# Performance work log

Hardware: AMD Instinct MI355X
Metric: run time of the kernel (lower is better)

The kernel has to match this reference:

```python
import jax, jax.numpy as jnp
import numpy as np

B, Z, D, V, IN, R = 4, 128, 2, 2, 512, 256


def setup_inputs() -> dict:
    key = jax.random.key(0)
    ks = jax.random.split(key, 9)
    scale = 1.0 / np.sqrt(IN)
    inp = {
        "x1": jax.random.normal(ks[0], (B, Z, D, V, IN), jnp.float32),
        "x2": jax.random.normal(ks[1], (B, Z, D, V, IN), jnp.float32),
        "x3": jax.random.normal(ks[2], (B, Z, D, V, IN), jnp.float32),
        "W1": jax.random.normal(ks[3], (IN, R), jnp.float32) * scale,
        "b1": jax.random.normal(ks[4], (R,), jnp.float32) * scale,
        "W2": jax.random.normal(ks[5], (IN, R), jnp.float32) * scale,
        "b2": jax.random.normal(ks[6], (R,), jnp.float32) * scale,
        "W3": jax.random.normal(ks[7], (IN, R), jnp.float32) * scale,
        "b3": jax.random.normal(ks[8], (R,), jnp.float32) * scale,
    }
    return inp


def reference(x1, x2, x3, W1, b1, W2, b2, W3, b3):
    # Linear projections: [b, pos, d, v, in] @ [in, r] -> [b, pos, d, v, r]
    p1 = jnp.einsum('bzdvi,ir->bzdvr', x1, W1) + b1
    p2 = jnp.einsum('bxdvi,ir->bxdvr', x2, W2) + b2
    p3 = jnp.einsum('bcdvi,ir->bcdvr', x3, W3) + b3
    # Trilinear contraction over the factorized rank r, broadcasting over d, v
    return jnp.einsum('bzdve,bxdve,bcdve->bzxcdv', p1, p2, p3)
```

## Files before the change

### kernel.cpp

```cpp
#include <hip/hip_runtime.h>
#include <hip/hip_bf16.h>


typedef _Float16 f16;
typedef __attribute__((ext_vector_type(8)))  _Float16 f16x8;
typedef __attribute__((ext_vector_type(4)))  float    f32x4;
typedef __attribute__((ext_vector_type(16))) float    f32x16;

__global__ __launch_bounds__(256) void proj_kernel(
    const float* __restrict__ x1, const float* __restrict__ x2, const float* __restrict__ x3,
    const float* __restrict__ W1, const float* __restrict__ b1,
    const float* __restrict__ W2, const float* __restrict__ b2,
    const float* __restrict__ W3, const float* __restrict__ b3,
    f16* __restrict__ p1, f16* __restrict__ p2, f16* __restrict__ p3) {
    const int mat = blockIdx.z;
    const float* __restrict__ x    = (mat == 0) ? x1 : (mat == 1) ? x2 : x3;
    const float* __restrict__ W    = (mat == 0) ? W1 : (mat == 1) ? W2 : W3;
    const float* __restrict__ bias = (mat == 0) ? b1 : (mat == 1) ? b2 : b3;
    f16* __restrict__ p = (mat == 0) ? p1 : (mat == 1) ? p2 : p3;

    const int tid  = threadIdx.x;
    const int lane = tid & 63;
    const int w    = tid >> 6;
    const int ln   = lane & 31;
    const int kq   = lane >> 5;
    const int m0   = blockIdx.x * 64 + (w >> 1) * 32;
    const int n0b  = blockIdx.y * 64;
    const int n0   = n0b + (w & 1) * 32;

    __shared__ f16 sWt[64 * 40];

    f32x16 acc;
#pragma unroll
    for (int i = 0; i < 16; ++i) acc[i] = 0.f;

    const int snn = tid & 63, skk0 = tid >> 6;

#pragma unroll 1
    for (int ch = 0; ch < 16; ++ch) {
        const int k0 = ch * 32;
#pragma unroll
        for (int j = 0; j < 8; ++j) {
            const int kk = skk0 + 4 * j;
            sWt[snn * 40 + kk] = (f16)W[(size_t)(k0 + kk) * 256 + n0b + snn];
        }
        __syncthreads();
#pragma unroll
        for (int ks = 0; ks < 2; ++ks) {
            const float* X = x + (size_t)(m0 + ln) * 512 + k0 + ks * 16 + kq * 8;
            f32x4 a0 = *(const f32x4*)X;
            f32x4 a1 = *(const f32x4*)(X + 4);
            f16x8 av;
            av[0] = (f16)a0[0]; av[1] = (f16)a0[1]; av[2] = (f16)a0[2]; av[3] = (f16)a0[3];
            av[4] = (f16)a1[0]; av[5] = (f16)a1[1]; av[6] = (f16)a1[2]; av[7] = (f16)a1[3];
            f16x8 bv = *(const f16x8*)&sWt[((w & 1) * 32 + ln) * 40 + ks * 16 + kq * 8];
            acc = __builtin_amdgcn_mfma_f32_32x32x16_f16(av, bv, acc, 0, 0, 0);
        }
        __syncthreads();
    }

    const int n = n0 + ln;
    const float bn = bias[n];
#pragma unroll
    for (int i = 0; i < 16; ++i) {
        const int m  = m0 + (i & 3) + 8 * (i >> 2) + 4 * kq;
        const int bb = m >> 9, z = (m >> 2) & 127, dv = m & 3;
        p[((bb * 4 + dv) * 128 + z) * 256 + n] = (f16)(acc[i] + bn);
    }
}

__global__ __launch_bounds__(256, 2) void tri_kernel(
    const f16* __restrict__ p1, const f16* __restrict__ p2,
    const f16* __restrict__ p3, float* __restrict__ out) {
    const int bi = blockIdx.x;
    const int zg = bi & 15;
    const int ct = (bi >> 4) & 3;
    const int xt = (bi >> 6) & 3;
    const int b  = bi >> 8;

    const int tid  = threadIdx.x;
    const int lane = tid & 63;
    const int w    = tid >> 6;
    const int ln   = lane & 31;
    const int kq   = lane >> 5;
    const int x0   = xt * 32;
    const int c0   = ct * 32;
    const int z0   = zg * 8;
    const int sl   = b * 4 + w;

    __shared__ __align__(16) f16  sP1[4][8 * 256];
    __shared__ float sT[4 * 32 * 33];

#pragma unroll
    for (int i = 0; i < 4; ++i) {
        const int G  = i * 64 + lane;
        const int zo = G >> 5, es = G & 31;
        f16x8 v = *(const f16x8*)(p1 + ((sl * 128 + z0 + zo) << 8) + es * 8);
        *(f16x8*)&sP1[w][G * 8] = v;
    }

    f16x8 pv[16], bq[16];
    const f16* P2r = p2 + ((sl * 128 + x0 + ln) << 8) + kq * 8;
    const f16* P3r = p3 + ((sl * 128 + c0 + ln) << 8) + kq * 8;
#pragma unroll
    for (int ks = 0; ks < 16; ++ks) {
        pv[ks] = *(const f16x8*)(P2r + ks * 16);
        bq[ks] = *(const f16x8*)(P3r + ks * 16);
    }

    const int cl = tid & 31, xg = tid >> 5;

#pragma unroll 1
    for (int zi = 0; zi < 8; ++zi) {
        f32x16 acc;
#pragma unroll
        for (int i = 0; i < 16; ++i) acc[i] = 0.f;

#pragma unroll
        for (int ks = 0; ks < 16; ++ks) {
            f16x8 u = *(const f16x8*)&sP1[w][(zi * 32 + ks * 2 + kq) * 8];
            f16x8 af = u * pv[ks];
            acc = __builtin_amdgcn_mfma_f32_32x32x16_f16(af, bq[ks], acc, 0, 0, 0);
        }

#pragma unroll
        for (int i = 0; i < 16; ++i) {
            const int xl = (i & 3) + 8 * (i >> 2) + 4 * kq;
            sT[w * 1056 + xl * 33 + ln] = acc[i];
        }
        __syncthreads();

        const int z = z0 + zi;
#pragma unroll
        for (int j = 0; j < 4; ++j) {
            const int xl = xg * 4 + j;
            f32x4 v;
            v[0] = sT[0 * 1056 + xl * 33 + cl];
            v[1] = sT[1 * 1056 + xl * 33 + cl];
            v[2] = sT[2 * 1056 + xl * 33 + cl];
            v[3] = sT[3 * 1056 + xl * 33 + cl];
            const size_t idx = (size_t)((b * 128 + z) * 128 + x0 + xl) * 128 + c0 + cl;
            *(f32x4*)(out + idx * 4) = v;
        }
        __syncthreads();
    }
}

extern "C" void kernel_launch(void* const* d_in, const int* in_sizes, int n_in,
                              void* d_out, int out_size, void* d_ws, size_t ws_size,
                              hipStream_t stream) {
    const float* x1 = (const float*)d_in[0];
    const float* x2 = (const float*)d_in[1];
    const float* x3 = (const float*)d_in[2];
    const float* W1 = (const float*)d_in[3];
    const float* b1 = (const float*)d_in[4];
    const float* W2 = (const float*)d_in[5];
    const float* b2 = (const float*)d_in[6];
    const float* W3 = (const float*)d_in[7];
    const float* b3 = (const float*)d_in[8];

    char* ws = (char*)d_ws;
    f16* p1 = (f16*)ws;
    f16* p2 = (f16*)(ws + (1u << 20));
    f16* p3 = (f16*)(ws + 2u * (1u << 20));

    proj_kernel<<<dim3(32, 4, 3), 256, 0, stream>>>(x1, x2, x3, W1, b1, W2, b2, W3, b3,
                                                    p1, p2, p3);
    tri_kernel<<<dim3(1024), 256, 0, stream>>>(p1, p2, p3, (float*)d_out);
}
```

Before: 62.59 us.

## Retile projection with 16x16 MFMA and read p1 directly in tri kernel

The projection kernel moves from 32x32x16 MFMA tiles over 64x64 blocks to 16x16x32 MFMA tiles over 64x16 blocks, launching four times as many blocks, and loads W with vectorized float4 reads. The trilinear kernel drops the shared-memory staging of p1 and reads it straight from global memory (all lanes of a half-wave hit the same address), which frees LDS so the occupancy hint can go from 2 to 3 blocks per CU. The intent is more parallelism in the projection and higher occupancy in the tri kernel. The cost is repeated global reads of the x inputs across the extra N-tiles, plus global-load latency inside the inner MFMA loop of the tri kernel.

```diff
diff --git a/kernel.cpp b/kernel.cpp
--- a/kernel.cpp
+++ b/kernel.cpp
@@ -22,54 +22,50 @@
     const int tid  = threadIdx.x;
     const int lane = tid & 63;
     const int w    = tid >> 6;
-    const int ln   = lane & 31;
-    const int kq   = lane >> 5;
-    const int m0   = blockIdx.x * 64 + (w >> 1) * 32;
-    const int n0b  = blockIdx.y * 64;
-    const int n0   = n0b + (w & 1) * 32;
+    const int ln   = lane & 15;
+    const int kq   = lane >> 4;
+    const int m0   = blockIdx.x * 64 + w * 16;
+    const int n0   = blockIdx.y * 16;
+    const int n    = n0 + ln;
 
-    __shared__ f16 sWt[64 * 40];
+    __shared__ f16 sWt[16 * 72];
 
-    f32x16 acc;
-#pragma unroll
-    for (int i = 0; i < 16; ++i) acc[i] = 0.f;
+    f32x4 acc = (f32x4){0.f, 0.f, 0.f, 0.f};
 
-    const int snn = tid & 63, skk0 = tid >> 6;
+    const int kk = tid >> 2, nq = tid & 3;
 
 #pragma unroll 1
-    for (int ch = 0; ch < 16; ++ch) {
-        const int k0 = ch * 32;
+    for (int ch = 0; ch < 8; ++ch) {
+        const int k0 = ch * 64;
+        f32x4 wv = *(const f32x4*)(W + (size_t)(k0 + kk) * 256 + n0 + nq * 4);
 #pragma unroll
-        for (int j = 0; j < 8; ++j) {
-            const int kk = skk0 + 4 * j;
-            sWt[snn * 40 + kk] = (f16)W[(size_t)(k0 + kk) * 256 + n0b + snn];
-        }
+        for (int i = 0; i < 4; ++i)
+            sWt[(nq * 4 + i) * 72 + kk] = (f16)wv[i];
         __syncthreads();
 #pragma unroll
-        for (int ks = 0; ks < 2; ++ks) {
-            const float* X = x + (size_t)(m0 + ln) * 512 + k0 + ks * 16 + kq * 8;
+        for (int kss = 0; kss < 2; ++kss) {
+            const float* X = x + (size_t)(m0 + ln) * 512 + k0 + kss * 32 + kq * 8;
             f32x4 a0 = *(const f32x4*)X;
             f32x4 a1 = *(const f32x4*)(X + 4);
             f16x8 av;
             av[0] = (f16)a0[0]; av[1] = (f16)a0[1]; av[2] = (f16)a0[2]; av[3] = (f16)a0[3];
             av[4] = (f16)a1[0]; av[5] = (f16)a1[1]; av[6] = (f16)a1[2]; av[7] = (f16)a1[3];
-            f16x8 bv = *(const f16x8*)&sWt[((w & 1) * 32 + ln) * 40 + ks * 16 + kq * 8];
-            acc = __builtin_amdgcn_mfma_f32_32x32x16_f16(av, bv, acc, 0, 0, 0);
+            f16x8 bv = *(const f16x8*)&sWt[ln * 72 + kss * 32 + kq * 8];
+            acc = __builtin_amdgcn_mfma_f32_16x16x32_f16(av, bv, acc, 0, 0, 0);
         }
         __syncthreads();
     }
 
-    const int n = n0 + ln;
     const float bn = bias[n];
 #pragma unroll
-    for (int i = 0; i < 16; ++i) {
-        const int m  = m0 + (i & 3) + 8 * (i >> 2) + 4 * kq;
+    for (int r = 0; r < 4; ++r) {
+        const int m  = m0 + kq * 4 + r;
         const int bb = m >> 9, z = (m >> 2) & 127, dv = m & 3;
-        p[((bb * 4 + dv) * 128 + z) * 256 + n] = (f16)(acc[i] + bn);
+        p[((bb * 4 + dv) * 128 + z) * 256 + n] = (f16)(acc[r] + bn);
     }
 }
 
-__global__ __launch_bounds__(256, 2) void tri_kernel(
+__global__ __launch_bounds__(256, 3) void tri_kernel(
     const f16* __restrict__ p1, const f16* __restrict__ p2,
     const f16* __restrict__ p3, float* __restrict__ out) {
     const int bi = blockIdx.x;
@@ -88,16 +84,7 @@
     const int z0   = zg * 8;
     const int sl   = b * 4 + w;
 
-    __shared__ __align__(16) f16  sP1[4][8 * 256];
     __shared__ float sT[4 * 32 * 33];
-
-#pragma unroll
-    for (int i = 0; i < 4; ++i) {
-        const int G  = i * 64 + lane;
-        const int zo = G >> 5, es = G & 31;
-        f16x8 v = *(const f16x8*)(p1 + ((sl * 128 + z0 + zo) << 8) + es * 8);
-        *(f16x8*)&sP1[w][G * 8] = v;
-    }
 
     f16x8 pv[16], bq[16];
     const f16* P2r = p2 + ((sl * 128 + x0 + ln) << 8) + kq * 8;
@@ -107,6 +94,7 @@
         pv[ks] = *(const f16x8*)(P2r + ks * 16);
         bq[ks] = *(const f16x8*)(P3r + ks * 16);
     }
+    const f16* P1r = p1 + ((sl * 128 + z0) << 8) + kq * 8;
 
     const int cl = tid & 31, xg = tid >> 5;
 
@@ -118,7 +106,7 @@
 
 #pragma unroll
         for (int ks = 0; ks < 16; ++ks) {
-            f16x8 u = *(const f16x8*)&sP1[w][(zi * 32 + ks * 2 + kq) * 8];
+            f16x8 u  = *(const f16x8*)(P1r + zi * 256 + ks * 16);
             f16x8 af = u * pv[ks];
             acc = __builtin_amdgcn_mfma_f32_32x32x16_f16(af, bq[ks], acc, 0, 0, 0);
         }
@@ -164,7 +152,7 @@
     f16* p2 = (f16*)(ws + (1u << 20));
     f16* p3 = (f16*)(ws + 2u * (1u << 20));
 
-    proj_kernel<<<dim3(32, 4, 3), 256, 0, stream>>>(x1, x2, x3, W1, b1, W2, b2, W3, b3,
-                                                    p1, p2, p3);
+    proj_kernel<<<dim3(32, 16, 3), 256, 0, stream>>>(x1, x2, x3, W1, b1, W2, b2, W3, b3,
+                                                     p1, p2, p3);
     tri_kernel<<<dim3(1024), 256, 0, stream>>>(p1, p2, p3, (float*)d_out);
 }
```

New measurement: 85.64 us. 1.37x slower.

## Double-buffer LDS in both kernels and prefetch next K-chunk in projection

Applied to the files above, without the earlier changes.

The projection kernel now prefetches the next chunk's W and x values into registers while the current chunk is computed. It also double-buffers the transposed W tile in LDS, so only one barrier per iteration is needed. The trilinear kernel double-buffers its output staging tile and replaces its two __syncthreads with a single custom barrier that waits only on LDS counters, letting global stores stay in flight across the barrier. This aims to hide load latency and cut barrier stalls, at the cost of more registers and LDS, which may lower occupancy.

```diff
diff --git a/kernel.cpp b/kernel.cpp
--- a/kernel.cpp
+++ b/kernel.cpp
@@ -6,6 +6,13 @@
 typedef __attribute__((ext_vector_type(8)))  _Float16 f16x8;
 typedef __attribute__((ext_vector_type(4)))  float    f32x4;
 typedef __attribute__((ext_vector_type(16))) float    f32x16;
+
+__device__ __forceinline__ void lds_barrier() {
+    __builtin_amdgcn_sched_barrier(0);
+    asm volatile("s_waitcnt lgkmcnt(0)" ::: "memory");
+    __builtin_amdgcn_s_barrier();
+    __builtin_amdgcn_sched_barrier(0);
+}
 
 __global__ __launch_bounds__(256) void proj_kernel(
     const float* __restrict__ x1, const float* __restrict__ x2, const float* __restrict__ x3,
@@ -28,35 +35,57 @@
     const int n0b  = blockIdx.y * 64;
     const int n0   = n0b + (w & 1) * 32;
 
-    __shared__ f16 sWt[64 * 40];
+    __shared__ f16 sWt[2][64 * 40];
 
     f32x16 acc;
 #pragma unroll
     for (int i = 0; i < 16; ++i) acc[i] = 0.f;
 
     const int snn = tid & 63, skk0 = tid >> 6;
+    const float* Xr = x + (size_t)(m0 + ln) * 512 + kq * 8;
+
+    float wr[8], wr2[8];
+    f32x4 xr[4], xn[4];
+#pragma unroll
+    for (int j = 0; j < 8; ++j)
+        wr[j] = W[(size_t)(skk0 + 4 * j) * 256 + n0b + snn];
+#pragma unroll
+    for (int t = 0; t < 2; ++t) {
+        xr[2 * t]     = *(const f32x4*)(Xr + t * 16);
+        xr[2 * t + 1] = *(const f32x4*)(Xr + t * 16 + 4);
+    }
 
 #pragma unroll 1
     for (int ch = 0; ch < 16; ++ch) {
-        const int k0 = ch * 32;
+        const int buf = ch & 1;
 #pragma unroll
-        for (int j = 0; j < 8; ++j) {
-            const int kk = skk0 + 4 * j;
-            sWt[snn * 40 + kk] = (f16)W[(size_t)(k0 + kk) * 256 + n0b + snn];
+        for (int j = 0; j < 8; ++j)
+            sWt[buf][snn * 40 + skk0 + 4 * j] = (f16)wr[j];
+        if (ch < 15) {
+            const int k1 = (ch + 1) * 32;
+#pragma unroll
+            for (int j = 0; j < 8; ++j)
+                wr2[j] = W[(size_t)(k1 + skk0 + 4 * j) * 256 + n0b + snn];
+#pragma unroll
+            for (int t = 0; t < 2; ++t) {
+                xn[2 * t]     = *(const f32x4*)(Xr + k1 + t * 16);
+                xn[2 * t + 1] = *(const f32x4*)(Xr + k1 + t * 16 + 4);
+            }
         }
-        __syncthreads();
+        lds_barrier();
 #pragma unroll
         for (int ks = 0; ks < 2; ++ks) {
-            const float* X = x + (size_t)(m0 + ln) * 512 + k0 + ks * 16 + kq * 8;
-            f32x4 a0 = *(const f32x4*)X;
-            f32x4 a1 = *(const f32x4*)(X + 4);
+            f32x4 a0 = xr[2 * ks], a1 = xr[2 * ks + 1];
             f16x8 av;
             av[0] = (f16)a0[0]; av[1] = (f16)a0[1]; av[2] = (f16)a0[2]; av[3] = (f16)a0[3];
             av[4] = (f16)a1[0]; av[5] = (f16)a1[1]; av[6] = (f16)a1[2]; av[7] = (f16)a1[3];
-            f16x8 bv = *(const f16x8*)&sWt[((w & 1) * 32 + ln) * 40 + ks * 16 + kq * 8];
+            f16x8 bv = *(const f16x8*)&sWt[buf][((w & 1) * 32 + ln) * 40 + ks * 16 + kq * 8];
             acc = __builtin_amdgcn_mfma_f32_32x32x16_f16(av, bv, acc, 0, 0, 0);
         }
-        __syncthreads();
+#pragma unroll
+        for (int t = 0; t < 4; ++t) xr[t] = xn[t];
+#pragma unroll
+        for (int j = 0; j < 8; ++j) wr[j] = wr2[j];
     }
 
     const int n = n0 + ln;
@@ -89,7 +118,7 @@
     const int sl   = b * 4 + w;
 
     __shared__ __align__(16) f16  sP1[4][8 * 256];
-    __shared__ float sT[4 * 32 * 33];
+    __shared__ float sT[2][4 * 32 * 33];
 
 #pragma unroll
     for (int i = 0; i < 4; ++i) {
@@ -123,26 +152,26 @@
             acc = __builtin_amdgcn_mfma_f32_32x32x16_f16(af, bq[ks], acc, 0, 0, 0);
         }
 
+        float* T = sT[zi & 1];
 #pragma unroll
         for (int i = 0; i < 16; ++i) {
             const int xl = (i & 3) + 8 * (i >> 2) + 4 * kq;
-            sT[w * 1056 + xl * 33 + ln] = acc[i];
+            T[w * 1056 + xl * 33 + ln] = acc[i];
         }
-        __syncthreads();
+        lds_barrier();
 
         const int z = z0 + zi;
 #pragma unroll
         for (int j = 0; j < 4; ++j) {
             const int xl = xg * 4 + j;
             f32x4 v;
-            v[0] = sT[0 * 1056 + xl * 33 + cl];
-            v[1] = sT[1 * 1056 + xl * 33 + cl];
-            v[2] = sT[2 * 1056 + xl * 33 + cl];
-            v[3] = sT[3 * 1056 + xl * 33 + cl];
+            v[0] = T[0 * 1056 + xl * 33 + cl];
+            v[1] = T[1 * 1056 + xl * 33 + cl];
+            v[2] = T[2 * 1056 + xl * 33 + cl];
+            v[3] = T[3 * 1056 + xl * 33 + cl];
             const size_t idx = (size_t)((b * 128 + z) * 128 + x0 + xl) * 128 + c0 + cl;
             *(f32x4*)(out + idx * 4) = v;
         }
-        __syncthreads();
     }
 }
 
```

New measurement: 57.61 us. 8.0% less time.
